# Kernel optimization log

Measured on AMD Instinct MI355X. Metric: run time of the kernel, lower is better.

Reference implementation:

```python
import jax, jax.numpy as jnp
import numpy as np

T = 0.07  # temperature from __init__ default


def setup_inputs() -> dict:
    key = jax.random.key(0)
    ks = jax.random.split(key, 5)
    B, D, H, E = 4096, 2048, 2048, 128
    init = lambda k, shp, fan: jax.random.normal(k, shp, dtype=jnp.float32) * (1.0 / np.sqrt(fan))
    return {
        "input1": jax.random.normal(ks[0], (B, D), dtype=jnp.float32),
        "input2": jax.random.normal(ks[1], (B, D), dtype=jnp.float32),
        "W0": init(ks[2], (D, H), D), "b0": jnp.zeros((H,), jnp.float32),
        "W1": init(ks[3], (H, H), H), "b1": jnp.zeros((H,), jnp.float32),
        "W2": init(ks[4], (H, E), H), "b2": jnp.zeros((E,), jnp.float32),
    }


def _mlp(x, W0, b0, W1, b1, W2, b2):
    # Linear -> ReLU -> Linear -> Linear (ReLU only between hidden layers)
    x = jax.nn.relu(x @ W0 + b0)
    x = x @ W1 + b1
    return x @ W2 + b2


def reference(input1, input2, W0, b0, W1, b1, W2, b2):
    B = input1.shape[0]
    e1 = _mlp(input1, W0, b0, W1, b1, W2, b2)
    e2 = _mlp(input2, W0, b0, W1, b1, W2, b2)
    feats = jnp.stack([e1, e2], axis=1)                       # [B, 2, E]
    feats = feats / jnp.linalg.norm(feats, axis=2, keepdims=True)
    # view(N,2,dim).permute(1,0,2).reshape(2N,dim): view0 rows then view1 rows
    f = jnp.concatenate([feats[:, 0], feats[:, 1]], axis=0)   # [2B, E]
    N2 = 2 * B
    sim = (f @ f.T) / T                                        # [2B, 2B]
    idx = jnp.arange(N2)
    pos = sim[idx, (idx + B) % N2]                             # partner view similarity
    # exclude self-similarity (diagonal) from the logsumexp denominator
    sim = jnp.where(jnp.eye(N2, dtype=bool), jnp.float32(-1e9), sim)
    # CE with positive at index 0 of [pos, negatives] == -pos + logsumexp(non-self)
    loss = jnp.mean(jax.nn.logsumexp(sim, axis=1) - pos)
    return loss
```

## Files before the change

kernel.cpp:

```cpp
#include <hip/hip_runtime.h>
#include <stdint.h>

typedef float f32x4 __attribute__((ext_vector_type(4)));
typedef float f32x16 __attribute__((ext_vector_type(16)));
typedef __bf16 bf16x8 __attribute__((ext_vector_type(8)));
typedef unsigned short u16;
typedef unsigned int u32;

#define INVT 14.285714285714286f
#define L2E  1.4426950408889634f

__device__ __forceinline__ u16 f2bf(float f) {
  u32 u = __float_as_uint(f);
  u32 r = (u + 0x7fffu + ((u >> 16) & 1u)) >> 16;
  return (u16)r;
}
__device__ __forceinline__ float bf2f(u16 h) { return __uint_as_float(((u32)h) << 16); }

__device__ __forceinline__ void g2l16(const void* g, void* l) {
  auto gp = reinterpret_cast<__attribute__((address_space(1))) uint32_t*>(
      reinterpret_cast<uintptr_t>(g));
  auto lp = reinterpret_cast<__attribute__((address_space(3))) uint32_t*>(
      reinterpret_cast<uintptr_t>(l));
  __builtin_amdgcn_global_load_lds(gp, lp, 16, 0, 0);
}

__global__ __launch_bounds__(256) void k_cvt2(const float* __restrict__ in1,
                                              const float* __restrict__ in2,
                                              u16* __restrict__ out) {
  int i = (blockIdx.x * 256 + threadIdx.x) * 4;
  float4 v;
  if (i < 8388608) v = *(const float4*)(in1 + i);
  else             v = *(const float4*)(in2 + (i - 8388608));
  ushort4 p;
  p.x = f2bf(v.x); p.y = f2bf(v.y); p.z = f2bf(v.z); p.w = f2bf(v.w);
  *(ushort4*)(out + i) = p;
}

__global__ __launch_bounds__(256) void k_transpose2(const float* __restrict__ w0,
                                                    u16* __restrict__ w0t,
                                                    const float* __restrict__ w1,
                                                    u16* __restrict__ w1t) {
  const float* in = blockIdx.z ? w1 : w0;
  u16* out = blockIdx.z ? w1t : w0t;
  const int R = 2048, C = 2048;
  __shared__ float t[64][65];
  const int r0 = blockIdx.y * 64, c0 = blockIdx.x * 64;
#pragma unroll
  for (int p = 0; p < 16; ++p) {
    int idx = p * 256 + threadIdx.x;
    int r = idx >> 6, c = idx & 63;
    t[r][c] = in[(size_t)(r0 + r) * C + (c0 + c)];
  }
  __syncthreads();
#pragma unroll
  for (int p = 0; p < 16; ++p) {
    int idx = p * 256 + threadIdx.x;
    int c = idx >> 6, r = idx & 63;
    out[(size_t)(c0 + c) * R + (r0 + r)] = f2bf(t[r][c]);
  }
}

__global__ __launch_bounds__(256) void k_transpose(const float* __restrict__ in,
                                                   u16* __restrict__ out, int R, int C) {
  __shared__ float t[64][65];
  const int r0 = blockIdx.y * 64, c0 = blockIdx.x * 64;
#pragma unroll
  for (int p = 0; p < 16; ++p) {
    int idx = p * 256 + threadIdx.x;
    int r = idx >> 6, c = idx & 63;
    t[r][c] = in[(size_t)(r0 + r) * C + (c0 + c)];
  }
  __syncthreads();
#pragma unroll
  for (int p = 0; p < 16; ++p) {
    int idx = p * 256 + threadIdx.x;
    int c = idx >> 6, r = idx & 63;
    out[(size_t)(c0 + c) * R + (r0 + r)] = f2bf(t[r][c]);
  }
}

__global__ __launch_bounds__(256, 1) void k_gemm(const u16* __restrict__ A, const u16* __restrict__ Bt,
                                                 const float* __restrict__ bias, u16* __restrict__ C,
                                                 int M, int N, int K, int relu) {
  __shared__ __align__(16) u16 sm[49152];
  const int tid = threadIdx.x;
  const int l = tid & 63, w = tid >> 6;
  const int wm = w >> 1, wn = w & 1;
  const int m0 = blockIdx.y * 256, n0 = blockIdx.x * 256;

  const int kb = ((l & 3) ^ ((l >> 3) & 3)) * 16;
  const char* gA = (const char*)(A + (size_t)(m0 + w * 64 + (l >> 2)) * K) + kb;
  const char* gB = (const char*)(Bt + (size_t)(n0 + w * 64 + (l >> 2)) * K) + kb;
  const size_t chRows = (size_t)16 * K * 2;

  auto issue = [&](int kcB, int stg) {
    char* base = (char*)sm + stg * 32768;
    char* dA = base + (w * 4) * 1024 + l * 16;
    char* dB = base + 16384 + (w * 4) * 1024 + l * 16;
#pragma unroll
    for (int j = 0; j < 4; ++j) g2l16(gA + j * chRows + kcB, dA + j * 1024);
#pragma unroll
    for (int j = 0; j < 4; ++j) g2l16(gB + j * chRows + kcB, dB + j * 1024);
  };

  const int lm = l & 31;
  const int c0 = l >> 5;
  const int sw = (lm >> 1) & 3;

  f32x16 acc[4][4] = {};

  auto compute = [&](int stg) {
    const u16* As = sm + stg * 16384;
    const u16* Bs = As + 8192;
#pragma unroll
    for (int t = 0; t < 2; ++t) {
      const int cc = (((t << 1) + c0) ^ sw) * 8;
      bf16x8 a4[4], b4[4];
#pragma unroll
      for (int fm = 0; fm < 4; ++fm)
        a4[fm] = *(const bf16x8*)(As + (wm * 128 + fm * 32 + lm) * 32 + cc);
#pragma unroll
      for (int fn = 0; fn < 4; ++fn)
        b4[fn] = *(const bf16x8*)(Bs + (wn * 128 + fn * 32 + lm) * 32 + cc);
#pragma unroll
      for (int fm = 0; fm < 4; ++fm)
#pragma unroll
        for (int fn = 0; fn < 4; ++fn)
          acc[fm][fn] = __builtin_amdgcn_mfma_f32_32x32x16_bf16(a4[fm], b4[fn],
                                                                acc[fm][fn], 0, 0, 0);
    }
  };

  const int NK = K >> 5;
  issue(0, 0);
  issue(64, 1);
  int st = 0;
  for (int kt = 0; kt < NK; ++kt) {
    if (kt + 1 < NK) asm volatile("s_waitcnt vmcnt(8)" ::: "memory");
    else             asm volatile("s_waitcnt vmcnt(0)" ::: "memory");
    asm volatile("s_barrier" ::: "memory");
    if (kt + 2 < NK) {
      int stp = st + 2; if (stp >= 3) stp -= 3;
      issue((kt + 2) * 64, stp);
    }
    compute(st);
    ++st; if (st == 3) st = 0;
  }

  const int colb = n0 + wn * 128 + lm;
  const int rowb = m0 + wm * 128 + 4 * c0;
#pragma unroll
  for (int fn = 0; fn < 4; ++fn) {
    const float b = bias[colb + fn * 32];
#pragma unroll
    for (int fm = 0; fm < 4; ++fm)
#pragma unroll
      for (int g = 0; g < 4; ++g)
#pragma unroll
        for (int rr = 0; rr < 4; ++rr) {
          float v = acc[fm][fn][g * 4 + rr] + b;
          if (relu) v = fmaxf(v, 0.0f);
          C[(size_t)(rowb + fm * 32 + g * 8 + rr) * N + colb + fn * 32] = f2bf(v);
        }
  }
}

__global__ __launch_bounds__(256, 2) void k_gemm_sk(const u16* __restrict__ A, const u16* __restrict__ Bt,
                                                    float* __restrict__ Ep, int K, int Ksplit) {
  __shared__ __align__(16) u16 sm[24576];
  const int tid = threadIdx.x;
  const int l = tid & 63, w = tid >> 6;
  const int wm = w >> 1, wn = w & 1;
  const int m0 = blockIdx.y * 128;
  const int split = blockIdx.x;
  const int k0s = split * Ksplit;

  const int kb = ((l & 3) ^ ((l >> 3) & 3)) * 16;
  const char* gA = (const char*)(A + (size_t)(m0 + w * 16 + (l >> 2)) * K + k0s) + kb;
  const char* gB = (const char*)(Bt + (size_t)(w * 16 + (l >> 2)) * K + k0s) + kb;
  const size_t radv = (size_t)64 * K * 2;

  auto issue = [&](int kcB, int stg) {
    char* base = (char*)sm + stg * 16384;
    char* dA = base + w * 1024 + l * 16;
    char* dB = base + 8192 + w * 1024 + l * 16;
    g2l16(gA + kcB, dA);
    g2l16(gA + radv + kcB, dA + 4096);
    g2l16(gB + kcB, dB);
    g2l16(gB + radv + kcB, dB + 4096);
  };

  const int lm = l & 31;
  const int c0 = l >> 5;
  const int sw = (lm >> 1) & 3;

  f32x16 acc[2][2] = {};

  auto compute = [&](int stg) {
    const u16* As = sm + stg * 8192;
    const u16* Bs = As + 4096;
#pragma unroll
    for (int t = 0; t < 2; ++t) {
      const int cc = (((t << 1) + c0) ^ sw) * 8;
      bf16x8 a2[2], b2[2];
#pragma unroll
      for (int fm = 0; fm < 2; ++fm) a2[fm] = *(const bf16x8*)(As + (wm * 64 + fm * 32 + lm) * 32 + cc);
#pragma unroll
      for (int fn = 0; fn < 2; ++fn) b2[fn] = *(const bf16x8*)(Bs + (wn * 64 + fn * 32 + lm) * 32 + cc);
#pragma unroll
      for (int fm = 0; fm < 2; ++fm)
#pragma unroll
        for (int fn = 0; fn < 2; ++fn)
          acc[fm][fn] = __builtin_amdgcn_mfma_f32_32x32x16_bf16(a2[fm], b2[fn],
                                                                acc[fm][fn], 0, 0, 0);
    }
  };

  const int NK = Ksplit >> 5;
  issue(0, 0);
  issue(64, 1);
  int st = 0;
  for (int kt = 0; kt < NK; ++kt) {
    if (kt + 1 < NK) asm volatile("s_waitcnt vmcnt(4)" ::: "memory");
    else             asm volatile("s_waitcnt vmcnt(0)" ::: "memory");
    asm volatile("s_barrier" ::: "memory");
    if (kt + 2 < NK) {
      int stp = st + 2; if (stp >= 3) stp -= 3;
      issue((kt + 2) * 64, stp);
    }
    compute(st);
    ++st; if (st == 3) st = 0;
  }

  const int colb = wn * 64 + lm;
  const int rowb = m0 + wm * 64 + 4 * c0;
#pragma unroll
  for (int fn = 0; fn < 2; ++fn)
#pragma unroll
    for (int fm = 0; fm < 2; ++fm)
#pragma unroll
      for (int g = 0; g < 4; ++g)
#pragma unroll
        for (int rr = 0; rr < 4; ++rr)
          Ep[((size_t)split * 8192 + rowb + fm * 32 + g * 8 + rr) * 128 + colb + fn * 32] =
              acc[fm][fn][g * 4 + rr];
}

__global__ __launch_bounds__(256) void k_norm(const float* __restrict__ Ep,
                                              const float* __restrict__ b2, u16* __restrict__ F) {
  const int l = threadIdx.x & 63, w = threadIdx.x >> 6;
  const int row = blockIdx.x * 4 + w;
  const float2* base = (const float2*)Ep + (size_t)row * 64 + l;
  float x = 0.f, y = 0.f;
#pragma unroll
  for (int s = 0; s < 4; ++s) {
    float2 t = base[(size_t)s * (8192 * 64)];
    x += t.x; y += t.y;
  }
  x += b2[l * 2]; y += b2[l * 2 + 1];
  float sq = x * x + y * y;
#pragma unroll
  for (int off = 1; off < 64; off <<= 1) sq += __shfl_xor(sq, off);
  const float inv = 1.0f / sqrtf(sq);
  F[(size_t)row * 128 + l * 2] = f2bf(x * inv);
  F[(size_t)row * 128 + l * 2 + 1] = f2bf(y * inv);
}

__global__ __launch_bounds__(256, 2) void k_sim(const u16* __restrict__ F, float* __restrict__ Sp) {
  __shared__ __align__(16) u16 sm[32768];
  const int tid = threadIdx.x;
  const int l = tid & 63, w = tid >> 6;
  const int wm = w >> 1, wn = w & 1;
  const int lm = l & 31, c0 = l >> 5;
  const int r0 = blockIdx.y * 128;
  const int cb0 = blockIdx.x * 1024;

  u16* B0 = sm;
  u16* AB1 = sm + 16384;

  const int srow0 = tid >> 4;
  const int schunk = tid & 15;
  auto stage = [&](const u16* src, u16* dst) {
#pragma unroll
    for (int j = 0; j < 8; ++j) {
      const int row = j * 16 + srow0;
      const int lc = schunk ^ (row & 7);
      g2l16((const char*)(src + (size_t)row * 128) + lc * 16,
            (char*)dst + j * 4096 + tid * 16);
    }
  };

  stage(F + (size_t)r0 * 128, AB1);
  asm volatile("s_waitcnt vmcnt(0)" ::: "memory");
  __syncthreads();

  bf16x8 a[2][8];
#pragma unroll
  for (int fm = 0; fm < 2; ++fm) {
    const int ra = wm * 64 + fm * 32 + lm;
#pragma unroll
    for (int kf = 0; kf < 8; ++kf)
      a[fm][kf] = *(const bf16x8*)(AB1 + ra * 128 + (((kf << 1) + c0) ^ (ra & 7)) * 8);
  }
  asm volatile("s_waitcnt lgkmcnt(0)" ::: "memory");

  stage(F + (size_t)cb0 * 128, B0);

  const float S2 = INVT * L2E;
  const int rB = wn * 64 + lm;
  f32x16 runS[2] = {};

#pragma unroll 1
  for (int p = 0; p < 8; ++p) {
    asm volatile("s_waitcnt vmcnt(0)" ::: "memory");
    asm volatile("s_barrier" ::: "memory");
    if (p < 7) stage(F + (size_t)(cb0 + (p + 1) * 128) * 128, (p & 1) ? B0 : AB1);
    const u16* Bs = (p & 1) ? AB1 : B0;

    f32x16 acc[2][2] = {};
#pragma unroll
    for (int kf = 0; kf < 8; ++kf) {
      const int kc = (kf << 1) + c0;
      bf16x8 b0v = *(const bf16x8*)(Bs + rB * 128 + (kc ^ (rB & 7)) * 8);
      bf16x8 b1v = *(const bf16x8*)(Bs + (rB + 32) * 128 + (kc ^ ((rB + 32) & 7)) * 8);
      acc[0][0] = __builtin_amdgcn_mfma_f32_32x32x16_bf16(a[0][kf], b0v, acc[0][0], 0, 0, 0);
      acc[0][1] = __builtin_amdgcn_mfma_f32_32x32x16_bf16(a[0][kf], b1v, acc[0][1], 0, 0, 0);
      acc[1][0] = __builtin_amdgcn_mfma_f32_32x32x16_bf16(a[1][kf], b0v, acc[1][0], 0, 0, 0);
      acc[1][1] = __builtin_amdgcn_mfma_f32_32x32x16_bf16(a[1][kf], b1v, acc[1][1], 0, 0, 0);
    }

    const int cp = cb0 + p * 128;
    if (cp == r0) {
#pragma unroll
      for (int fm = 0; fm < 2; ++fm)
#pragma unroll
        for (int fn = 0; fn < 2; ++fn) {
          const int rcol = wn * 64 + fn * 32 + lm;
#pragma unroll
          for (int r = 0; r < 16; ++r) {
            const int rrow = wm * 64 + fm * 32 + (r & 3) + 8 * (r >> 2) + 4 * c0;
            float e = exp2f(fmaf(acc[fm][fn][r], S2, -S2));
            if (rrow == rcol) e = 0.f;
            runS[fm][r] += e;
          }
        }
    } else {
#pragma unroll
      for (int fm = 0; fm < 2; ++fm)
#pragma unroll
        for (int fn = 0; fn < 2; ++fn)
#pragma unroll
          for (int r = 0; r < 16; ++r)
            runS[fm][r] += exp2f(fmaf(acc[fm][fn][r], S2, -S2));
    }
  }

#pragma unroll
  for (int fm = 0; fm < 2; ++fm)
#pragma unroll
    for (int r = 0; r < 16; ++r) {
      float s = runS[fm][r];
      s += __shfl_xor(s, 1);
      s += __shfl_xor(s, 2);
      s += __shfl_xor(s, 4);
      s += __shfl_xor(s, 8);
      s += __shfl_xor(s, 16);
      runS[fm][r] = s;
    }

  __syncthreads();
  float* red = (float*)sm;
  if (wn == 0) {
    if (lm == 0) {
#pragma unroll
      for (int fm = 0; fm < 2; ++fm)
#pragma unroll
        for (int r = 0; r < 16; ++r)
          red[wm * 64 + fm * 32 + (r & 3) + 8 * (r >> 2) + 4 * c0] = runS[fm][r];
    }
  }
  __syncthreads();
  if (wn == 1 && lm == 0) {
#pragma unroll
    for (int fm = 0; fm < 2; ++fm)
#pragma unroll
      for (int r = 0; r < 16; ++r) {
        const int rr = wm * 64 + fm * 32 + (r & 3) + 8 * (r >> 2) + 4 * c0;
        Sp[(size_t)blockIdx.x * 8192 + r0 + rr] = red[rr] + runS[fm][r];
      }
  }
}

__global__ __launch_bounds__(256) void k_combine(const float* __restrict__ Sp,
                                                 const u16* __restrict__ F,
                                                 float* __restrict__ out) {
  const int r = blockIdx.x * 256 + threadIdx.x;
  float S = 0.f;
#pragma unroll
  for (int c = 0; c < 8; ++c) S += Sp[c * 8192 + r];
  const float lse = INVT + logf(S);
  const int par = (r + 4096) & 8191;
  const u16* a = F + (size_t)r * 128;
  const u16* b = F + (size_t)par * 128;
  float dot = 0.f;
#pragma unroll 8
  for (int k = 0; k < 128; ++k) dot = fmaf(bf2f(a[k]), bf2f(b[k]), dot);
  float contrib = lse - dot * INVT;
#pragma unroll
  for (int off = 1; off < 64; off <<= 1) contrib += __shfl_xor(contrib, off);
  if ((threadIdx.x & 63) == 0) atomicAdd(out, contrib * (1.0f / 8192.0f));
}

extern "C" void kernel_launch(void* const* d_in, const int* in_sizes, int n_in,
                              void* d_out, int out_size, void* d_ws, size_t ws_size,
                              hipStream_t stream) {
  const float* input1 = (const float*)d_in[0];
  const float* input2 = (const float*)d_in[1];
  const float* W0 = (const float*)d_in[2];
  const float* b0 = (const float*)d_in[3];
  const float* W1 = (const float*)d_in[4];
  const float* b1 = (const float*)d_in[5];
  const float* W2 = (const float*)d_in[6];
  const float* b2 = (const float*)d_in[7];
  float* out = (float*)d_out;
  char* ws = (char*)d_ws;

  u16* Xb = (u16*)(ws + 0);
  u16* H1 = (u16*)(ws + 33554432);
  u16* W0T = (u16*)(ws + 67108864);
  u16* W1T = (u16*)(ws + 75497472);
  float* Ep = (float*)(ws + 67108864);
  u16* W2T = (u16*)(ws + 83886080);
  float* Sp = (float*)(ws + 83886080);
  u16* Ff = (u16*)(ws + 84410368);
  u16* H2 = Xb;

  hipMemsetAsync(d_out, 0, sizeof(float), stream);
  k_cvt2<<<16384, 256, 0, stream>>>(input1, input2, Xb);
  k_transpose2<<<dim3(32, 32, 2), 256, 0, stream>>>(W0, W0T, W1, W1T);
  k_transpose<<<dim3(2, 32), 256, 0, stream>>>(W2, W2T, 2048, 128);
  k_gemm<<<dim3(8, 32), 256, 0, stream>>>(Xb, W0T, b0, H1, 8192, 2048, 2048, 1);
  k_gemm<<<dim3(8, 32), 256, 0, stream>>>(H1, W1T, b1, H2, 8192, 2048, 2048, 0);
  k_gemm_sk<<<dim3(4, 64), 256, 0, stream>>>(H2, W2T, Ep, 2048, 512);
  k_norm<<<2048, 256, 0, stream>>>(Ep, b2, Ff);
  k_sim<<<dim3(8, 64), 256, 0, stream>>>(Ff, Sp);
  k_combine<<<32, 256, 0, stream>>>(Sp, Ff, out);
}
```

Measured before the change: 353.6 us.

## Retile big GEMMs to 256x128 two-wave blocks and fuse final layer with normalization

The large GEMMs move from 256x256 tiles with 4 waves to 256x128 tiles with 2 waves. This doubles the grid to 512 blocks to fill more CUs, and the loader now issues 12 loads per wave. The split-K final projection and the separate norm kernel are replaced by one k_embed kernel. It computes 16 rows x 128 columns per block with 16x16 MFMAs reading straight from global memory, then adds the bias, normalizes and writes bf16. This removes the fp32 partial-sum round trip and a launch, but the GEMM waves now carry more work each, and k_embed has no LDS reuse of W2T.

```diff
diff --git a/kernel.cpp b/kernel.cpp
--- a/kernel.cpp
+++ b/kernel.cpp
@@ -80,28 +80,28 @@
   }
 }
 
-__global__ __launch_bounds__(256, 1) void k_gemm(const u16* __restrict__ A, const u16* __restrict__ Bt,
+__global__ __launch_bounds__(128, 1) void k_gemm(const u16* __restrict__ A, const u16* __restrict__ Bt,
                                                  const float* __restrict__ bias, u16* __restrict__ C,
                                                  int M, int N, int K, int relu) {
-  __shared__ __align__(16) u16 sm[49152];
+  __shared__ __align__(16) u16 sm[36864];
   const int tid = threadIdx.x;
-  const int l = tid & 63, w = tid >> 6;
-  const int wm = w >> 1, wn = w & 1;
-  const int m0 = blockIdx.y * 256, n0 = blockIdx.x * 256;
+  const int l = tid & 63, w2 = tid >> 6;
+  const int m0 = blockIdx.y * 256, n0 = blockIdx.x * 128;
 
   const int kb = ((l & 3) ^ ((l >> 3) & 3)) * 16;
-  const char* gA = (const char*)(A + (size_t)(m0 + w * 64 + (l >> 2)) * K) + kb;
-  const char* gB = (const char*)(Bt + (size_t)(n0 + w * 64 + (l >> 2)) * K) + kb;
+  const char* gA = (const char*)(A + (size_t)(m0 + (l >> 2)) * K) + kb;
+  const char* gB = (const char*)(Bt + (size_t)(n0 + (l >> 2)) * K) + kb;
   const size_t chRows = (size_t)16 * K * 2;
 
   auto issue = [&](int kcB, int stg) {
-    char* base = (char*)sm + stg * 32768;
-    char* dA = base + (w * 4) * 1024 + l * 16;
-    char* dB = base + 16384 + (w * 4) * 1024 + l * 16;
-#pragma unroll
-    for (int j = 0; j < 4; ++j) g2l16(gA + j * chRows + kcB, dA + j * 1024);
-#pragma unroll
-    for (int j = 0; j < 4; ++j) g2l16(gB + j * chRows + kcB, dB + j * 1024);
+    char* dst = (char*)sm + stg * 24576 + (w2 * 12) * 1024 + l * 16;
+#pragma unroll
+    for (int j = 0; j < 12; ++j) {
+      const int c = w2 * 12 + j;
+      const char* s = (c < 16) ? (gA + (size_t)c * chRows + kcB)
+                               : (gB + (size_t)(c - 16) * chRows + kcB);
+      g2l16(s, dst + j * 1024);
+    }
   };
 
   const int lm = l & 31;
@@ -111,7 +111,7 @@
   f32x16 acc[4][4] = {};
 
   auto compute = [&](int stg) {
-    const u16* As = sm + stg * 16384;
+    const u16* As = sm + stg * 12288;
     const u16* Bs = As + 8192;
 #pragma unroll
     for (int t = 0; t < 2; ++t) {
@@ -119,10 +119,10 @@
       bf16x8 a4[4], b4[4];
 #pragma unroll
       for (int fm = 0; fm < 4; ++fm)
-        a4[fm] = *(const bf16x8*)(As + (wm * 128 + fm * 32 + lm) * 32 + cc);
+        a4[fm] = *(const bf16x8*)(As + (w2 * 128 + fm * 32 + lm) * 32 + cc);
 #pragma unroll
       for (int fn = 0; fn < 4; ++fn)
-        b4[fn] = *(const bf16x8*)(Bs + (wn * 128 + fn * 32 + lm) * 32 + cc);
+        b4[fn] = *(const bf16x8*)(Bs + (fn * 32 + lm) * 32 + cc);
 #pragma unroll
       for (int fm = 0; fm < 4; ++fm)
 #pragma unroll
@@ -137,7 +137,7 @@
   issue(64, 1);
   int st = 0;
   for (int kt = 0; kt < NK; ++kt) {
-    if (kt + 1 < NK) asm volatile("s_waitcnt vmcnt(8)" ::: "memory");
+    if (kt + 1 < NK) asm volatile("s_waitcnt vmcnt(12)" ::: "memory");
     else             asm volatile("s_waitcnt vmcnt(0)" ::: "memory");
     asm volatile("s_barrier" ::: "memory");
     if (kt + 2 < NK) {
@@ -148,8 +148,8 @@
     ++st; if (st == 3) st = 0;
   }
 
-  const int colb = n0 + wn * 128 + lm;
-  const int rowb = m0 + wm * 128 + 4 * c0;
+  const int colb = n0 + lm;
+  const int rowb = m0 + w2 * 128 + 4 * c0;
 #pragma unroll
   for (int fn = 0; fn < 4; ++fn) {
     const float b = bias[colb + fn * 32];
@@ -166,105 +166,53 @@
   }
 }
 
-__global__ __launch_bounds__(256, 2) void k_gemm_sk(const u16* __restrict__ A, const u16* __restrict__ Bt,
-                                                    float* __restrict__ Ep, int K, int Ksplit) {
-  __shared__ __align__(16) u16 sm[24576];
+__global__ __launch_bounds__(256, 2) void k_embed(const u16* __restrict__ H, const u16* __restrict__ Bt,
+                                                  const float* __restrict__ b2, u16* __restrict__ F) {
   const int tid = threadIdx.x;
   const int l = tid & 63, w = tid >> 6;
-  const int wm = w >> 1, wn = w & 1;
-  const int m0 = blockIdx.y * 128;
-  const int split = blockIdx.x;
-  const int k0s = split * Ksplit;
-
-  const int kb = ((l & 3) ^ ((l >> 3) & 3)) * 16;
-  const char* gA = (const char*)(A + (size_t)(m0 + w * 16 + (l >> 2)) * K + k0s) + kb;
-  const char* gB = (const char*)(Bt + (size_t)(w * 16 + (l >> 2)) * K + k0s) + kb;
-  const size_t radv = (size_t)64 * K * 2;
-
-  auto issue = [&](int kcB, int stg) {
-    char* base = (char*)sm + stg * 16384;
-    char* dA = base + w * 1024 + l * 16;
-    char* dB = base + 8192 + w * 1024 + l * 16;
-    g2l16(gA + kcB, dA);
-    g2l16(gA + radv + kcB, dA + 4096);
-    g2l16(gB + kcB, dB);
-    g2l16(gB + radv + kcB, dB + 4096);
-  };
-
-  const int lm = l & 31;
-  const int c0 = l >> 5;
-  const int sw = (lm >> 1) & 3;
-
-  f32x16 acc[2][2] = {};
-
-  auto compute = [&](int stg) {
-    const u16* As = sm + stg * 8192;
-    const u16* Bs = As + 4096;
-#pragma unroll
-    for (int t = 0; t < 2; ++t) {
-      const int cc = (((t << 1) + c0) ^ sw) * 8;
-      bf16x8 a2[2], b2[2];
-#pragma unroll
-      for (int fm = 0; fm < 2; ++fm) a2[fm] = *(const bf16x8*)(As + (wm * 64 + fm * 32 + lm) * 32 + cc);
-#pragma unroll
-      for (int fn = 0; fn < 2; ++fn) b2[fn] = *(const bf16x8*)(Bs + (wn * 64 + fn * 32 + lm) * 32 + cc);
-#pragma unroll
-      for (int fm = 0; fm < 2; ++fm)
-#pragma unroll
-        for (int fn = 0; fn < 2; ++fn)
-          acc[fm][fn] = __builtin_amdgcn_mfma_f32_32x32x16_bf16(a2[fm], b2[fn],
-                                                                acc[fm][fn], 0, 0, 0);
-    }
-  };
-
-  const int NK = Ksplit >> 5;
-  issue(0, 0);
-  issue(64, 1);
-  int st = 0;
-  for (int kt = 0; kt < NK; ++kt) {
-    if (kt + 1 < NK) asm volatile("s_waitcnt vmcnt(4)" ::: "memory");
-    else             asm volatile("s_waitcnt vmcnt(0)" ::: "memory");
-    asm volatile("s_barrier" ::: "memory");
-    if (kt + 2 < NK) {
-      int stp = st + 2; if (stp >= 3) stp -= 3;
-      issue((kt + 2) * 64, stp);
-    }
-    compute(st);
-    ++st; if (st == 3) st = 0;
-  }
-
-  const int colb = wn * 64 + lm;
-  const int rowb = m0 + wm * 64 + 4 * c0;
-#pragma unroll
-  for (int fn = 0; fn < 2; ++fn)
-#pragma unroll
-    for (int fm = 0; fm < 2; ++fm)
-#pragma unroll
-      for (int g = 0; g < 4; ++g)
-#pragma unroll
-        for (int rr = 0; rr < 4; ++rr)
-          Ep[((size_t)split * 8192 + rowb + fm * 32 + g * 8 + rr) * 128 + colb + fn * 32] =
-              acc[fm][fn][g * 4 + rr];
-}
-
-__global__ __launch_bounds__(256) void k_norm(const float* __restrict__ Ep,
-                                              const float* __restrict__ b2, u16* __restrict__ F) {
-  const int l = threadIdx.x & 63, w = threadIdx.x >> 6;
-  const int row = blockIdx.x * 4 + w;
-  const float2* base = (const float2*)Ep + (size_t)row * 64 + l;
-  float x = 0.f, y = 0.f;
-#pragma unroll
-  for (int s = 0; s < 4; ++s) {
-    float2 t = base[(size_t)s * (8192 * 64)];
-    x += t.x; y += t.y;
-  }
-  x += b2[l * 2]; y += b2[l * 2 + 1];
-  float sq = x * x + y * y;
-#pragma unroll
-  for (int off = 1; off < 64; off <<= 1) sq += __shfl_xor(sq, off);
-  const float inv = 1.0f / sqrtf(sq);
-  F[(size_t)row * 128 + l * 2] = f2bf(x * inv);
-  F[(size_t)row * 128 + l * 2 + 1] = f2bf(y * inv);
+  const int m = l & 15, kq = l >> 4;
+  const int r0 = blockIdx.x * 16;
+
+  const char* pA = (const char*)(H + (size_t)(r0 + m) * 2048) + kq * 16;
+  const char* pB0 = (const char*)(Bt + (size_t)(w * 32 + m) * 2048) + kq * 16;
+  const char* pB1 = pB0 + (size_t)16 * 2048 * 2;
+
+  f32x4 acc0 = {}, acc1 = {};
+#pragma unroll 8
+  for (int k = 0; k < 64; ++k) {
+    bf16x8 av = *(const bf16x8*)(pA + k * 64);
+    bf16x8 b0 = *(const bf16x8*)(pB0 + k * 64);
+    bf16x8 b1 = *(const bf16x8*)(pB1 + k * 64);
+    acc0 = __builtin_amdgcn_mfma_f32_16x16x32_bf16(av, b0, acc0, 0, 0, 0);
+    acc1 = __builtin_amdgcn_mfma_f32_16x16x32_bf16(av, b1, acc1, 0, 0, 0);
+  }
+
+  const float vb0 = b2[w * 32 + m], vb1 = b2[w * 32 + 16 + m];
+  float v0[4], v1[4], s[4];
+#pragma unroll
+  for (int r = 0; r < 4; ++r) {
+    v0[r] = acc0[r] + vb0;
+    v1[r] = acc1[r] + vb1;
+    s[r] = v0[r] * v0[r] + v1[r] * v1[r];
+  }
+#pragma unroll
+  for (int off = 1; off < 16; off <<= 1)
+#pragma unroll
+    for (int r = 0; r < 4; ++r) s[r] += __shfl_xor(s[r], off);
+
+  __shared__ float red[4][16];
+  if (m == 0) {
+#pragma unroll
+    for (int r = 0; r < 4; ++r) red[w][kq * 4 + r] = s[r];
+  }
+  __syncthreads();
+#pragma unroll
+  for (int r = 0; r < 4; ++r) {
+    const int row = kq * 4 + r;
+    const float inv = rsqrtf(red[0][row] + red[1][row] + red[2][row] + red[3][row]);
+    F[(size_t)(r0 + row) * 128 + w * 32 + m] = f2bf(v0[r] * inv);
+    F[(size_t)(r0 + row) * 128 + w * 32 + 16 + m] = f2bf(v1[r] * inv);
+  }
 }
 
 __global__ __launch_bounds__(256, 2) void k_sim(const u16* __restrict__ F, float* __restrict__ Sp) {
@@ -430,7 +378,6 @@
   u16* H1 = (u16*)(ws + 33554432);
   u16* W0T = (u16*)(ws + 67108864);
   u16* W1T = (u16*)(ws + 75497472);
-  float* Ep = (float*)(ws + 67108864);
   u16* W2T = (u16*)(ws + 83886080);
   float* Sp = (float*)(ws + 83886080);
   u16* Ff = (u16*)(ws + 84410368);
@@ -440,10 +387,9 @@
   k_cvt2<<<16384, 256, 0, stream>>>(input1, input2, Xb);
   k_transpose2<<<dim3(32, 32, 2), 256, 0, stream>>>(W0, W0T, W1, W1T);
   k_transpose<<<dim3(2, 32), 256, 0, stream>>>(W2, W2T, 2048, 128);
-  k_gemm<<<dim3(8, 32), 256, 0, stream>>>(Xb, W0T, b0, H1, 8192, 2048, 2048, 1);
-  k_gemm<<<dim3(8, 32), 256, 0, stream>>>(H1, W1T, b1, H2, 8192, 2048, 2048, 0);
-  k_gemm_sk<<<dim3(4, 64), 256, 0, stream>>>(H2, W2T, Ep, 2048, 512);
-  k_norm<<<2048, 256, 0, stream>>>(Ep, b2, Ff);
+  k_gemm<<<dim3(16, 32), 128, 0, stream>>>(Xb, W0T, b0, H1, 8192, 2048, 2048, 1);
+  k_gemm<<<dim3(16, 32), 128, 0, stream>>>(H1, W1T, b1, H2, 8192, 2048, 2048, 0);
+  k_embed<<<512, 256, 0, stream>>>(H2, W2T, b2, Ff);
   k_sim<<<dim3(8, 64), 256, 0, stream>>>(Ff, Sp);
   k_combine<<<32, 256, 0, stream>>>(Sp, Ff, out);
 }
```

Result: slower. 382.1 us (+8.1%).
